# Optimization experiments

Measured on AMD Instinct MI355X. Metric: run time of the kernel, lower is better.

Reference implementation:

```python
import jax, jax.numpy as jnp
import numpy as np

NUM_LEVELS = 8
BASE_RES = 16
MAX_RES = 1024
TABLE_SIZE = 2 ** 17
FEAT = 2
ALPHA_SHIFT = 5.0
ALPHA_SCALE = 1.0

_growth = np.exp((np.log(MAX_RES) - np.log(BASE_RES)) / (NUM_LEVELS - 1))
SCALINGS = np.floor(BASE_RES * _growth ** np.arange(NUM_LEVELS)).astype(np.float32)  # per-level grid res
CORNERS = np.array([[(i >> 2) & 1, (i >> 1) & 1, i & 1] for i in range(8)], dtype=np.int32)  # voxel corners
PRIMES = np.array([1, 2654435761, 805459861], dtype=np.uint32)  # nerfstudio hash primes


def hash_encode(pos, table):
    # pos: [N,3] in [0,1]; table: [NUM_LEVELS*TABLE_SIZE, FEAT]
    scaled = pos[:, None, :] * jnp.asarray(SCALINGS)[None, :, None]              # [N,L,3]
    f = jnp.floor(scaled)
    w = scaled - f                                                               # trilinear weights
    idx = f.astype(jnp.int32)[:, :, None, :] + jnp.asarray(CORNERS)[None, None]  # [N,L,8,3]
    h = idx.astype(jnp.uint32) * jnp.asarray(PRIMES)
    hashed = (h[..., 0] ^ h[..., 1] ^ h[..., 2]) % TABLE_SIZE                    # [N,L,8]
    hashed = hashed.astype(jnp.int32) + (jnp.arange(NUM_LEVELS, dtype=jnp.int32) * TABLE_SIZE)[None, :, None]
    feats = table[hashed]                                                        # [N,L,8,F] gather
    cw = jnp.where(jnp.asarray(CORNERS)[None, None] == 1, w[:, :, None, :], 1.0 - w[:, :, None, :]).prod(-1)
    out = (feats * cw[..., None]).sum(2)                                         # [N,L,F]
    return out.reshape(pos.shape[0], NUM_LEVELS * FEAT)


def setup_inputs():
    key = jax.random.key(0)
    ks = jax.random.split(key, 8)
    R, S = 8192, 48
    return {
        "positions": jax.random.normal(ks[0], (R, S, 3), jnp.float32),
        "c2ws": jax.random.normal(ks[1], (R, 3, 4), jnp.float32) * 0.5,
        "aabb": jnp.array([[-1.0, -1.0, -1.0], [1.0, 1.0, 1.0]], jnp.float32),
        "table": jax.random.uniform(ks[2], (NUM_LEVELS * TABLE_SIZE, FEAT), jnp.float32, -1e-4, 1e-4),
        "w1": jax.random.normal(ks[3], (16, 32), jnp.float32) * 0.25,
        "b1": jnp.zeros((32,), jnp.float32),
        "w2": jax.random.normal(ks[4], (32, 16), jnp.float32) * 0.18,
        "b2": jnp.zeros((16,), jnp.float32),
        "hw1": jax.random.normal(ks[5], (16, 64), jnp.float32) * 0.25,
        "hb1": jnp.zeros((64,), jnp.float32),
        "hw2": jax.random.normal(ks[6], (64, 1), jnp.float32) * 0.125,
        "hb2": jnp.zeros((1,), jnp.float32),
    }


def reference(positions, c2ws, aabb, table, w1, b1, w2, b2, hw1, hb1, hw2, hb2):
    R, S = positions.shape[:2]
    rot = c2ws[:, :3, :3]
    trans = c2ws[:, :3, 3]
    rot_t = jnp.swapaxes(rot, 1, 2)                          # w2c rotation = R^T
    t_w2c = -jnp.einsum('rij,rj->ri', rot_t, trans)          # w2c translation = -R^T t
    pos = jnp.einsum('rij,rsj->rsi', rot_t, positions) + t_w2c[:, None, :]
    pos = (pos - aabb[0]) / (aabb[1] - aabb[0])              # SceneBox.get_normalized_positions
    selector = jnp.all((pos > 0.0) & (pos < 1.0), axis=-1)   # inside unit cube
    pos = pos * selector[..., None]
    enc = hash_encode(pos.reshape(-1, 3), table)             # [N, 16]
    h = jax.nn.relu(enc @ w1 + b1) @ w2 + b2                 # mlp_base -> geo features
    o = jax.nn.relu(h @ hw1 + hb1) @ hw2 + hb2               # mlp_head -> alpha logits
    o = o.reshape(R, S, -1)
    return ALPHA_SCALE * jax.nn.sigmoid(o - ALPHA_SHIFT) * selector[..., None]
```

## Files before the change

### kernel.cpp

```cpp
#include <hip/hip_runtime.h>
#include <math.h>
#include <stdint.h>

#define NLEV 8
#define TSIZE 131072
#define TMASK (TSIZE - 1)

__global__ __launch_bounds__(256) void rif_kernel(
    const float* __restrict__ positions,
    const float* __restrict__ c2ws,
    const float* __restrict__ aabb,
    const float* __restrict__ table,
    const float* __restrict__ w1, const float* __restrict__ b1,
    const float* __restrict__ w2, const float* __restrict__ b2,
    const float* __restrict__ hw1, const float* __restrict__ hb1,
    const float* __restrict__ hw2, const float* __restrict__ hb2,
    float* __restrict__ out, int total, int S)
{
    __shared__ float sw1[512];
    __shared__ float sb1[32];
    __shared__ float sw2[512];
    __shared__ float sb2[16];
    __shared__ float shw1[1024];
    __shared__ float shb1[64];
    __shared__ float shw2[64];
    __shared__ float shb2[1];

    for (int i = threadIdx.x; i < 512; i += 256) { sw1[i] = w1[i]; sw2[i] = w2[i]; }
    for (int i = threadIdx.x; i < 1024; i += 256) shw1[i] = hw1[i];
    if (threadIdx.x < 64) { shb1[threadIdx.x] = hb1[threadIdx.x]; shw2[threadIdx.x] = hw2[threadIdx.x]; }
    if (threadIdx.x < 32) sb1[threadIdx.x] = b1[threadIdx.x];
    if (threadIdx.x < 16) sb2[threadIdx.x] = b2[threadIdx.x];
    if (threadIdx.x == 0) shb2[0] = hb2[0];
    __syncthreads();

    int gid = blockIdx.x * blockDim.x + threadIdx.x;
    if (gid >= total) return;
    int r = gid / S;

    const float* p = positions + (size_t)gid * 3;
    const float* c = c2ws + (size_t)r * 12;
    float px = p[0], py = p[1], pz = p[2];
    float c00 = c[0], c01 = c[1], c02 = c[2],  t0 = c[3];
    float c10 = c[4], c11 = c[5], c12 = c[6],  t1 = c[7];
    float c20 = c[8], c21 = c[9], c22 = c[10], t2 = c[11];

    float m0 = __fadd_rn(__fadd_rn(__fmul_rn(c00, px), __fmul_rn(c10, py)), __fmul_rn(c20, pz));
    float m1 = __fadd_rn(__fadd_rn(__fmul_rn(c01, px), __fmul_rn(c11, py)), __fmul_rn(c21, pz));
    float m2 = __fadd_rn(__fadd_rn(__fmul_rn(c02, px), __fmul_rn(c12, py)), __fmul_rn(c22, pz));
    float n0 = __fadd_rn(__fadd_rn(__fmul_rn(c00, t0), __fmul_rn(c10, t1)), __fmul_rn(c20, t2));
    float n1 = __fadd_rn(__fadd_rn(__fmul_rn(c01, t0), __fmul_rn(c11, t1)), __fmul_rn(c21, t2));
    float n2 = __fadd_rn(__fadd_rn(__fmul_rn(c02, t0), __fmul_rn(c12, t1)), __fmul_rn(c22, t2));
    float posx = __fsub_rn(m0, n0);
    float posy = __fsub_rn(m1, n1);
    float posz = __fsub_rn(m2, n2);

    float a0x = aabb[0], a0y = aabb[1], a0z = aabb[2];
    float a1x = aabb[3], a1y = aabb[4], a1z = aabb[5];
    posx = __fdiv_rn(__fsub_rn(posx, a0x), __fsub_rn(a1x, a0x));
    posy = __fdiv_rn(__fsub_rn(posy, a0y), __fsub_rn(a1y, a0y));
    posz = __fdiv_rn(__fsub_rn(posz, a0z), __fsub_rn(a1z, a0z));

    bool sel = (posx > 0.f) & (posx < 1.f) & (posy > 0.f) & (posy < 1.f) & (posz > 0.f) & (posz < 1.f);
    if (!sel) { out[gid] = 0.f; return; }

    const float kScale[8] = {16.f, 28.f, 52.f, 95.f, 172.f, 312.f, 565.f, 1024.f};
    float enc[16];
    #pragma unroll
    for (int l = 0; l < NLEV; ++l) {
        float sc = kScale[l];
        float sx = posx * sc, sy = posy * sc, sz = posz * sc;
        float fx = floorf(sx), fy = floorf(sy), fz = floorf(sz);
        float wx = sx - fx, wy = sy - fy, wz = sz - fz;
        uint32_t ix = (uint32_t)(int)fx, iy = (uint32_t)(int)fy, iz = (uint32_t)(int)fz;
        uint32_t hy0 = iy * 2654435761u, hy1 = hy0 + 2654435761u;
        uint32_t hz0 = iz * 805459861u,  hz1 = hz0 + 805459861u;
        const float2* tab = (const float2*)table + (size_t)l * TSIZE;
        float f0 = 0.f, f1 = 0.f;
        #pragma unroll
        for (int cc = 0; cc < 8; ++cc) {
            uint32_t cx = (cc >> 2) & 1, cy = (cc >> 1) & 1, cz = cc & 1;
            uint32_t hh = ((ix + cx) ^ (cy ? hy1 : hy0) ^ (cz ? hz1 : hz0)) & TMASK;
            float wgt = (cx ? wx : 1.f - wx) * (cy ? wy : 1.f - wy) * (cz ? wz : 1.f - wz);
            float2 ft = tab[hh];
            f0 = fmaf(ft.x, wgt, f0);
            f1 = fmaf(ft.y, wgt, f1);
        }
        enc[2 * l] = f0;
        enc[2 * l + 1] = f1;
    }

    float h1[32];
    #pragma unroll
    for (int j = 0; j < 32; ++j) h1[j] = sb1[j];
    #pragma unroll
    for (int i = 0; i < 16; ++i) {
        float e = enc[i];
        #pragma unroll
        for (int j = 0; j < 32; ++j) h1[j] = fmaf(e, sw1[i * 32 + j], h1[j]);
    }
    #pragma unroll
    for (int j = 0; j < 32; ++j) h1[j] = fmaxf(h1[j], 0.f);

    float h2[16];
    #pragma unroll
    for (int j = 0; j < 16; ++j) h2[j] = sb2[j];
    #pragma unroll
    for (int i = 0; i < 32; ++i) {
        float e = h1[i];
        #pragma unroll
        for (int j = 0; j < 16; ++j) h2[j] = fmaf(e, sw2[i * 16 + j], h2[j]);
    }

    float o = shb2[0];
    #pragma unroll
    for (int j = 0; j < 64; ++j) {
        float acc = shb1[j];
        #pragma unroll
        for (int i = 0; i < 16; ++i) acc = fmaf(h2[i], shw1[i * 64 + j], acc);
        o = fmaf(fmaxf(acc, 0.f), shw2[j], o);
    }

    float x = o - 5.0f;
    out[gid] = 1.0f / (1.0f + expf(-x));
}

extern "C" void kernel_launch(void* const* d_in, const int* in_sizes, int n_in,
                              void* d_out, int out_size, void* d_ws, size_t ws_size,
                              hipStream_t stream) {
    const float* positions = (const float*)d_in[0];
    const float* c2ws      = (const float*)d_in[1];
    const float* aabb      = (const float*)d_in[2];
    const float* table     = (const float*)d_in[3];
    const float* w1  = (const float*)d_in[4];
    const float* b1  = (const float*)d_in[5];
    const float* w2  = (const float*)d_in[6];
    const float* b2  = (const float*)d_in[7];
    const float* hw1 = (const float*)d_in[8];
    const float* hb1 = (const float*)d_in[9];
    const float* hw2 = (const float*)d_in[10];
    const float* hb2 = (const float*)d_in[11];

    int R = in_sizes[1] / 12;
    int total = in_sizes[0] / 3;
    int S = total / R;

    int threads = 256;
    int blocks = (total + threads - 1) / threads;
    hipLaunchKernelGGL(rif_kernel, dim3(blocks), dim3(threads), 0, stream,
                       positions, c2ws, aabb, table,
                       w1, b1, w2, b2, hw1, hb1, hw2, hb2,
                       (float*)d_out, total, S);
}
```

Baseline: 74.08 us.

## Compact in-box samples per block and batch hash gathers across levels

Uses a wave ballot and a block prefix sum to pack the samples that fall inside the box into the lowest threads, so the hash encoding and MLP run on dense waves instead of divergent ones. Table gathers for four levels at a time are issued before any weighting, with a scheduling barrier, so more loads are in flight at once. MLP weights are now read through scalar or constant loads instead of being staged in LDS, and launch bounds request two blocks. Costs are three extra syncthreads, more registers held by the batched gathers, and a scattered output write.

```diff
diff --git a/kernel.cpp b/kernel.cpp
--- a/kernel.cpp
+++ b/kernel.cpp
@@ -6,7 +6,7 @@
 #define TSIZE 131072
 #define TMASK (TSIZE - 1)
 
-__global__ __launch_bounds__(256) void rif_kernel(
+__global__ __launch_bounds__(256, 2) void rif_fused(
     const float* __restrict__ positions,
     const float* __restrict__ c2ws,
     const float* __restrict__ aabb,
@@ -17,112 +17,150 @@
     const float* __restrict__ hw2, const float* __restrict__ hb2,
     float* __restrict__ out, int total, int S)
 {
-    __shared__ float sw1[512];
-    __shared__ float sb1[32];
-    __shared__ float sw2[512];
-    __shared__ float sb2[16];
-    __shared__ float shw1[1024];
-    __shared__ float shb1[64];
-    __shared__ float shw2[64];
-    __shared__ float shb2[1];
+    __shared__ float sPX[256], sPY[256], sPZ[256];
+    __shared__ int   sIdx[256];
+    __shared__ int   wbase[4];
+    __shared__ int   sCnt;
 
-    for (int i = threadIdx.x; i < 512; i += 256) { sw1[i] = w1[i]; sw2[i] = w2[i]; }
-    for (int i = threadIdx.x; i < 1024; i += 256) shw1[i] = hw1[i];
-    if (threadIdx.x < 64) { shb1[threadIdx.x] = hb1[threadIdx.x]; shw2[threadIdx.x] = hw2[threadIdx.x]; }
-    if (threadIdx.x < 32) sb1[threadIdx.x] = b1[threadIdx.x];
-    if (threadIdx.x < 16) sb2[threadIdx.x] = b2[threadIdx.x];
-    if (threadIdx.x == 0) shb2[0] = hb2[0];
+    int gid = blockIdx.x * 256 + threadIdx.x;
+    bool inRange = gid < total;
+
+    float posx = 0.f, posy = 0.f, posz = 0.f;
+    bool sel = false;
+    if (inRange) {
+        int r = gid / S;
+        const float* p = positions + (size_t)gid * 3;
+        const float* c = c2ws + (size_t)r * 12;
+        float px = p[0], py = p[1], pz = p[2];
+        float c00 = c[0], c01 = c[1], c02 = c[2],  t0 = c[3];
+        float c10 = c[4], c11 = c[5], c12 = c[6],  t1 = c[7];
+        float c20 = c[8], c21 = c[9], c22 = c[10], t2 = c[11];
+
+        float m0 = __fadd_rn(__fadd_rn(__fmul_rn(c00, px), __fmul_rn(c10, py)), __fmul_rn(c20, pz));
+        float m1 = __fadd_rn(__fadd_rn(__fmul_rn(c01, px), __fmul_rn(c11, py)), __fmul_rn(c21, pz));
+        float m2 = __fadd_rn(__fadd_rn(__fmul_rn(c02, px), __fmul_rn(c12, py)), __fmul_rn(c22, pz));
+        float n0 = __fadd_rn(__fadd_rn(__fmul_rn(c00, t0), __fmul_rn(c10, t1)), __fmul_rn(c20, t2));
+        float n1 = __fadd_rn(__fadd_rn(__fmul_rn(c01, t0), __fmul_rn(c11, t1)), __fmul_rn(c21, t2));
+        float n2 = __fadd_rn(__fadd_rn(__fmul_rn(c02, t0), __fmul_rn(c12, t1)), __fmul_rn(c22, t2));
+        float x0 = __fsub_rn(m0, n0);
+        float x1 = __fsub_rn(m1, n1);
+        float x2 = __fsub_rn(m2, n2);
+
+        float a0x = aabb[0], a0y = aabb[1], a0z = aabb[2];
+        float a1x = aabb[3], a1y = aabb[4], a1z = aabb[5];
+        posx = __fdiv_rn(__fsub_rn(x0, a0x), __fsub_rn(a1x, a0x));
+        posy = __fdiv_rn(__fsub_rn(x1, a0y), __fsub_rn(a1y, a0y));
+        posz = __fdiv_rn(__fsub_rn(x2, a0z), __fsub_rn(a1z, a0z));
+        sel = (posx > 0.f) & (posx < 1.f) & (posy > 0.f) & (posy < 1.f) & (posz > 0.f) & (posz < 1.f);
+        if (!sel) out[gid] = 0.f;
+    }
+
+    unsigned long long m = __ballot(sel);
+    int lane = threadIdx.x & 63;
+    int wid  = threadIdx.x >> 6;
+    int pre  = __popcll(m & ((1ull << lane) - 1ull));
+    if (lane == 0) wbase[wid] = __popcll(m);
+    __syncthreads();
+    if (threadIdx.x == 0) {
+        int s = 0;
+        #pragma unroll
+        for (int w = 0; w < 4; ++w) { int t = wbase[w]; wbase[w] = s; s += t; }
+        sCnt = s;
+    }
+    __syncthreads();
+    if (sel) {
+        int slot = wbase[wid] + pre;
+        sIdx[slot] = threadIdx.x;
+        sPX[slot] = posx; sPY[slot] = posy; sPZ[slot] = posz;
+    }
     __syncthreads();
 
-    int gid = blockIdx.x * blockDim.x + threadIdx.x;
-    if (gid >= total) return;
-    int r = gid / S;
+    int cnt = sCnt;
+    int t = threadIdx.x;
+    if (t >= cnt) return;
 
-    const float* p = positions + (size_t)gid * 3;
-    const float* c = c2ws + (size_t)r * 12;
-    float px = p[0], py = p[1], pz = p[2];
-    float c00 = c[0], c01 = c[1], c02 = c[2],  t0 = c[3];
-    float c10 = c[4], c11 = c[5], c12 = c[6],  t1 = c[7];
-    float c20 = c[8], c21 = c[9], c22 = c[10], t2 = c[11];
-
-    float m0 = __fadd_rn(__fadd_rn(__fmul_rn(c00, px), __fmul_rn(c10, py)), __fmul_rn(c20, pz));
-    float m1 = __fadd_rn(__fadd_rn(__fmul_rn(c01, px), __fmul_rn(c11, py)), __fmul_rn(c21, pz));
-    float m2 = __fadd_rn(__fadd_rn(__fmul_rn(c02, px), __fmul_rn(c12, py)), __fmul_rn(c22, pz));
-    float n0 = __fadd_rn(__fadd_rn(__fmul_rn(c00, t0), __fmul_rn(c10, t1)), __fmul_rn(c20, t2));
-    float n1 = __fadd_rn(__fadd_rn(__fmul_rn(c01, t0), __fmul_rn(c11, t1)), __fmul_rn(c21, t2));
-    float n2 = __fadd_rn(__fadd_rn(__fmul_rn(c02, t0), __fmul_rn(c12, t1)), __fmul_rn(c22, t2));
-    float posx = __fsub_rn(m0, n0);
-    float posy = __fsub_rn(m1, n1);
-    float posz = __fsub_rn(m2, n2);
-
-    float a0x = aabb[0], a0y = aabb[1], a0z = aabb[2];
-    float a1x = aabb[3], a1y = aabb[4], a1z = aabb[5];
-    posx = __fdiv_rn(__fsub_rn(posx, a0x), __fsub_rn(a1x, a0x));
-    posy = __fdiv_rn(__fsub_rn(posy, a0y), __fsub_rn(a1y, a0y));
-    posz = __fdiv_rn(__fsub_rn(posz, a0z), __fsub_rn(a1z, a0z));
-
-    bool sel = (posx > 0.f) & (posx < 1.f) & (posy > 0.f) & (posy < 1.f) & (posz > 0.f) & (posz < 1.f);
-    if (!sel) { out[gid] = 0.f; return; }
+    posx = sPX[t]; posy = sPY[t]; posz = sPZ[t];
+    int ogid = blockIdx.x * 256 + sIdx[t];
 
     const float kScale[8] = {16.f, 28.f, 52.f, 95.f, 172.f, 312.f, 565.f, 1024.f};
     float enc[16];
+
     #pragma unroll
-    for (int l = 0; l < NLEV; ++l) {
-        float sc = kScale[l];
-        float sx = posx * sc, sy = posy * sc, sz = posz * sc;
-        float fx = floorf(sx), fy = floorf(sy), fz = floorf(sz);
-        float wx = sx - fx, wy = sy - fy, wz = sz - fz;
-        uint32_t ix = (uint32_t)(int)fx, iy = (uint32_t)(int)fy, iz = (uint32_t)(int)fz;
-        uint32_t hy0 = iy * 2654435761u, hy1 = hy0 + 2654435761u;
-        uint32_t hz0 = iz * 805459861u,  hz1 = hz0 + 805459861u;
-        const float2* tab = (const float2*)table + (size_t)l * TSIZE;
-        float f0 = 0.f, f1 = 0.f;
+    for (int half = 0; half < 2; ++half) {
+        float wxs[4], wys[4], wzs[4];
+        float2 ft[4][8];
         #pragma unroll
-        for (int cc = 0; cc < 8; ++cc) {
-            uint32_t cx = (cc >> 2) & 1, cy = (cc >> 1) & 1, cz = cc & 1;
-            uint32_t hh = ((ix + cx) ^ (cy ? hy1 : hy0) ^ (cz ? hz1 : hz0)) & TMASK;
-            float wgt = (cx ? wx : 1.f - wx) * (cy ? wy : 1.f - wy) * (cz ? wz : 1.f - wz);
-            float2 ft = tab[hh];
-            f0 = fmaf(ft.x, wgt, f0);
-            f1 = fmaf(ft.y, wgt, f1);
+        for (int l4 = 0; l4 < 4; ++l4) {
+            int l = half * 4 + l4;
+            float sc = kScale[l];
+            float sx = posx * sc, sy = posy * sc, sz = posz * sc;
+            float fx = floorf(sx), fy = floorf(sy), fz = floorf(sz);
+            wxs[l4] = sx - fx; wys[l4] = sy - fy; wzs[l4] = sz - fz;
+            uint32_t ix = (uint32_t)(int)fx, iy = (uint32_t)(int)fy, iz = (uint32_t)(int)fz;
+            uint32_t hy0 = iy * 2654435761u, hy1 = hy0 + 2654435761u;
+            uint32_t hz0 = iz * 805459861u,  hz1 = hz0 + 805459861u;
+            const float2* tab = (const float2*)table + (size_t)l * TSIZE;
+            #pragma unroll
+            for (int cc = 0; cc < 8; ++cc) {
+                uint32_t cx = (cc >> 2) & 1, cy = (cc >> 1) & 1, cz = cc & 1;
+                uint32_t hh = ((ix + cx) ^ (cy ? hy1 : hy0) ^ (cz ? hz1 : hz0)) & TMASK;
+                ft[l4][cc] = tab[hh];
+            }
         }
-        enc[2 * l] = f0;
-        enc[2 * l + 1] = f1;
+        __builtin_amdgcn_sched_barrier(0);
+        #pragma unroll
+        for (int l4 = 0; l4 < 4; ++l4) {
+            int l = half * 4 + l4;
+            float wx = wxs[l4], wy = wys[l4], wz = wzs[l4];
+            float ux = 1.f - wx, uy = 1.f - wy, uz = 1.f - wz;
+            float q00 = uy * uz, q01 = uy * wz, q10 = wy * uz, q11 = wy * wz;
+            float f0, f1;
+            f0 = ft[l4][0].x * (ux * q00); f1 = ft[l4][0].y * (ux * q00);
+            f0 = fmaf(ft[l4][1].x, ux * q01, f0); f1 = fmaf(ft[l4][1].y, ux * q01, f1);
+            f0 = fmaf(ft[l4][2].x, ux * q10, f0); f1 = fmaf(ft[l4][2].y, ux * q10, f1);
+            f0 = fmaf(ft[l4][3].x, ux * q11, f0); f1 = fmaf(ft[l4][3].y, ux * q11, f1);
+            f0 = fmaf(ft[l4][4].x, wx * q00, f0); f1 = fmaf(ft[l4][4].y, wx * q00, f1);
+            f0 = fmaf(ft[l4][5].x, wx * q01, f0); f1 = fmaf(ft[l4][5].y, wx * q01, f1);
+            f0 = fmaf(ft[l4][6].x, wx * q10, f0); f1 = fmaf(ft[l4][6].y, wx * q10, f1);
+            f0 = fmaf(ft[l4][7].x, wx * q11, f0); f1 = fmaf(ft[l4][7].y, wx * q11, f1);
+            enc[2 * l] = f0;
+            enc[2 * l + 1] = f1;
+        }
     }
 
     float h1[32];
     #pragma unroll
-    for (int j = 0; j < 32; ++j) h1[j] = sb1[j];
+    for (int j = 0; j < 32; ++j) h1[j] = b1[j];
     #pragma unroll
     for (int i = 0; i < 16; ++i) {
         float e = enc[i];
         #pragma unroll
-        for (int j = 0; j < 32; ++j) h1[j] = fmaf(e, sw1[i * 32 + j], h1[j]);
+        for (int j = 0; j < 32; ++j) h1[j] = fmaf(e, w1[i * 32 + j], h1[j]);
     }
     #pragma unroll
     for (int j = 0; j < 32; ++j) h1[j] = fmaxf(h1[j], 0.f);
 
     float h2[16];
     #pragma unroll
-    for (int j = 0; j < 16; ++j) h2[j] = sb2[j];
+    for (int j = 0; j < 16; ++j) h2[j] = b2[j];
     #pragma unroll
     for (int i = 0; i < 32; ++i) {
         float e = h1[i];
         #pragma unroll
-        for (int j = 0; j < 16; ++j) h2[j] = fmaf(e, sw2[i * 16 + j], h2[j]);
+        for (int j = 0; j < 16; ++j) h2[j] = fmaf(e, w2[i * 16 + j], h2[j]);
     }
 
-    float o = shb2[0];
+    float o = hb2[0];
     #pragma unroll
     for (int j = 0; j < 64; ++j) {
-        float acc = shb1[j];
+        float acc = hb1[j];
         #pragma unroll
-        for (int i = 0; i < 16; ++i) acc = fmaf(h2[i], shw1[i * 64 + j], acc);
-        o = fmaf(fmaxf(acc, 0.f), shw2[j], o);
+        for (int i = 0; i < 16; ++i) acc = fmaf(h2[i], hw1[i * 64 + j], acc);
+        o = fmaf(fmaxf(acc, 0.f), hw2[j], o);
     }
 
     float x = o - 5.0f;
-    out[gid] = 1.0f / (1.0f + expf(-x));
+    out[ogid] = 1.0f / (1.0f + expf(-x));
 }
 
 extern "C" void kernel_launch(void* const* d_in, const int* in_sizes, int n_in,
@@ -147,7 +185,7 @@
 
     int threads = 256;
     int blocks = (total + threads - 1) / threads;
-    hipLaunchKernelGGL(rif_kernel, dim3(blocks), dim3(threads), 0, stream,
+    hipLaunchKernelGGL(rif_fused, dim3(blocks), dim3(threads), 0, stream,
                        positions, c2ws, aabb, table,
                        w1, b1, w2, b2, hw1, hb1, hw2, hb2,
                        (float*)d_out, total, S);
```

Measured after the change: 73.15 us. About the same (-1.3%).
